# Optimization experiments

Hardware: AMD Instinct MI355X
Metric: run time of the kernel (lower is better)

Reference implementation:

```python
import jax, jax.numpy as jnp
import numpy as np

# dims
B, N, C_A, C_S, C_Z = 2, 8192, 128, 384, 16
H, D = 4, 32            # n_heads, head_dim (H*D == C_A)
NQ, NK = 32, 128        # local window: queries / keys
NB = 3                  # n_blocks
W = N // NQ             # number of query windows
HID = 2 * C_A           # transition expansion (n=2)


def _ln(x, eps=1e-5):
    # LayerNorm without affine params
    m = jnp.mean(x, axis=-1, keepdims=True)
    v = jnp.var(x, axis=-1, keepdims=True)
    return (x - m) * jax.lax.rsqrt(v + eps)


def setup_inputs() -> dict:
    key = jax.random.key(0)
    ks = iter(jax.random.split(key, 40))
    def rn(shape, scale=1.0):
        return jax.random.normal(next(ks), shape, dtype=jnp.float32) * jnp.float32(scale)
    inp = {
        'q': rn((B, N, C_A)),
        's': rn((B, N, C_S)),
        'p': rn((B, W, NQ, NK, C_Z)),
        # AttentionPairBias (AF3 Alg 24) params, stacked over blocks
        'adaln_scale_w': rn((NB, C_S, C_A), C_S ** -0.5),
        'adaln_scale_b': jnp.zeros((NB, C_A), jnp.float32),
        'adaln_shift_w': rn((NB, C_S, C_A), C_S ** -0.5),
        'wq': rn((NB, C_A, H * D), C_A ** -0.5),
        'bq': jnp.zeros((NB, H * D), jnp.float32),
        'wk': rn((NB, C_A, H * D), C_A ** -0.5),
        'wv': rn((NB, C_A, H * D), C_A ** -0.5),
        'lnz_w': jnp.ones((NB, C_Z), jnp.float32),
        'lnz_b': jnp.zeros((NB, C_Z), jnp.float32),
        'wb_pair': rn((NB, C_Z, H), C_Z ** -0.5),
        'wg': rn((NB, C_A, H * D), C_A ** -0.5),
        'wo': rn((NB, H * D, C_A), (H * D) ** -0.5),
        'sgate_w': rn((NB, C_S, C_A), C_S ** -0.5),
        'sgate_b': jnp.full((NB, C_A), -2.0, jnp.float32),
        # ConditionedTransitionBlock (AF3 Alg 25) params
        't_scale_w': rn((NB, C_S, C_A), C_S ** -0.5),
        't_scale_b': jnp.zeros((NB, C_A), jnp.float32),
        't_shift_w': rn((NB, C_S, C_A), C_S ** -0.5),
        't_wa': rn((NB, C_A, HID), C_A ** -0.5),
        't_wb': rn((NB, C_A, HID), C_A ** -0.5),
        't_wo': rn((NB, HID, C_A), HID ** -0.5),
        't_sgate_w': rn((NB, C_S, C_A), C_S ** -0.5),
        't_sgate_b': jnp.full((NB, C_A), -2.0, jnp.float32),
    }
    return inp


def reference(q, s, p,
              adaln_scale_w, adaln_scale_b, adaln_shift_w,
              wq, bq, wk, wv, lnz_w, lnz_b, wb_pair, wg, wo, sgate_w, sgate_b,
              t_scale_w, t_scale_b, t_shift_w, t_wa, t_wb, t_wo, t_sgate_w, t_sgate_b):
    a = q
    s_ln = _ln(s)  # [B, N, C_S], shared across blocks
    # local window key indices: window w covers queries [w*NQ, (w+1)*NQ), keys
    # are a centered NK-wide window -> offsets in [-(NK-NQ)//2, ...)
    off = (NK - NQ) // 2
    idx = jnp.arange(W)[:, None] * NQ - off + jnp.arange(NK)[None, :]  # [W, NK]
    valid = (idx >= 0) & (idx < N)
    idx_c = jnp.clip(idx, 0, N - 1)
    inv_sqrt_d = jnp.float32(1.0 / np.sqrt(D))
    NEG = jnp.float32(-1e9)

    for i in range(NB):
        # ---- AttentionPairBias (AdaLN-conditioned, pair-biased, gated) ----
        a_ln = _ln(a)
        a_ln = jax.nn.sigmoid(s_ln @ adaln_scale_w[i] + adaln_scale_b[i]) * a_ln \
               + s_ln @ adaln_shift_w[i]
        qh = (a_ln @ wq[i] + bq[i]).reshape(B, N, H, D)
        kh = (a_ln @ wk[i]).reshape(B, N, H, D)
        vh = (a_ln @ wv[i]).reshape(B, N, H, D)
        g = jax.nn.sigmoid(a_ln @ wg[i]).reshape(B, N, H, D)
        # pair bias from z: LN + linear to heads -> [B, W, NQ, NK, H]
        bias = (_ln(p) * lnz_w[i] + lnz_b[i]) @ wb_pair[i]
        qw = qh.reshape(B, W, NQ, H, D)
        kw = kh[:, idx_c]  # [B, W, NK, H, D]
        vw = vh[:, idx_c]
        logits = jnp.einsum('bwqhd,bwkhd->bwqkh', qw, kw) * inv_sqrt_d + bias
        logits = jnp.where(valid[None, :, None, :, None], logits, NEG)
        attn = jax.nn.softmax(logits, axis=3)
        ow = jnp.einsum('bwqkh,bwkhd->bwqhd', attn, vw)
        o = (g * ow.reshape(B, N, H, D)).reshape(B, N, H * D)
        attn_out = (o @ wo[i]) * jax.nn.sigmoid(s_ln @ sgate_w[i] + sgate_b[i])
        # ---- ConditionedTransitionBlock (SwiGLU, sigmoid-gated) ----
        t_ln = _ln(a)
        t_ln = jax.nn.sigmoid(s_ln @ t_scale_w[i] + t_scale_b[i]) * t_ln \
               + s_ln @ t_shift_w[i]
        hidden = jax.nn.silu(t_ln @ t_wa[i]) * (t_ln @ t_wb[i])
        trans_out = (hidden @ t_wo[i]) * jax.nn.sigmoid(s_ln @ t_sgate_w[i] + t_sgate_b[i])
        # AF3 Alg 23: a <- b + ConditionedTransitionBlock(a, s)
        a = attn_out + trans_out
    return a
```

## Files before the change

kernel.cpp:

```cpp
#include <hip/hip_runtime.h>
#include <hip/hip_bf16.h>
#include <cstddef>
#include <cstdint>

#define BB   2
#define NN   8192
#define CA   128
#define CS   384
#define CZ   16
#define HH   4
#define DD   32
#define NQW  32
#define NKW  128
#define NBLK 3
#define WW   256
#define MR   (BB*NN)
#define HIDN 256

typedef unsigned short u16;
typedef __attribute__((ext_vector_type(8))) short short8;
typedef __attribute__((ext_vector_type(4))) float floatx4;

__device__ __forceinline__ float sigmoidf_(float x) { return 1.f / (1.f + __expf(-x)); }

__device__ __forceinline__ u16 f2bf(float x) {
  unsigned u = __float_as_uint(x);
  unsigned r = (u + 0x7fffu + ((u >> 16) & 1u)) >> 16;
  return (u16)r;
}
__device__ __forceinline__ float bf2f(u16 u) {
  return __uint_as_float(((unsigned)u) << 16);
}

__device__ __forceinline__ void gload16(const u16* g, u16* l) {
  __builtin_amdgcn_global_load_lds(
      (const __attribute__((address_space(1))) unsigned int*)g,
      (__attribute__((address_space(3))) unsigned int*)l, 16, 0, 0);
}

__global__ __launch_bounds__(256) void ln_s_kernel(const float* __restrict__ s,
                                                   u16* __restrict__ s_ln_bf) {
  int row  = blockIdx.x * 4 + (threadIdx.x >> 6);
  int lane = threadIdx.x & 63;
  const float* sr = s + (size_t)row * CS;
  float x[6];
  float sum = 0.f, sq = 0.f;
#pragma unroll
  for (int t = 0; t < 6; ++t) { x[t] = sr[lane + 64*t]; sum += x[t]; sq += x[t]*x[t]; }
#pragma unroll
  for (int off = 32; off; off >>= 1) { sum += __shfl_down(sum, off); sq += __shfl_down(sq, off); }
  sum = __shfl(sum, 0); sq = __shfl(sq, 0);
  float mean = sum * (1.f/CS);
  float var  = sq  * (1.f/CS) - mean*mean;
  float rstd = rsqrtf(var + 1e-5f);
  u16* orow = s_ln_bf + (size_t)row * CS;
#pragma unroll
  for (int t = 0; t < 6; ++t) orow[lane + 64*t] = f2bf((x[t]-mean)*rstd);
}

__global__ __launch_bounds__(256) void modln_kernel(const float* __restrict__ a,
                                                    const u16* __restrict__ sp0,
                                                    const u16* __restrict__ sp1,
                                                    const u16* __restrict__ sp3,
                                                    const u16* __restrict__ sp4,
                                                    u16* __restrict__ amod,
                                                    u16* __restrict__ tmod) {
  int row  = blockIdx.x * 4 + (threadIdx.x >> 6);
  int lane = threadIdx.x & 63;
  const float* ar = a + (size_t)row * CA;
  float x0 = ar[lane], x1 = ar[lane + 64];
  float sum = x0 + x1, sq = x0*x0 + x1*x1;
#pragma unroll
  for (int off = 32; off; off >>= 1) { sum += __shfl_down(sum, off); sq += __shfl_down(sq, off); }
  sum = __shfl(sum, 0); sq = __shfl(sq, 0);
  float mean = sum * (1.f/CA);
  float var  = sq  * (1.f/CA) - mean*mean;
  float rstd = rsqrtf(var + 1e-5f);
  float n0 = (x0-mean)*rstd, n1 = (x1-mean)*rstd;
  size_t i0 = (size_t)row * CA + lane;
  amod[i0]      = f2bf(bf2f(sp0[i0])     *n0 + bf2f(sp1[i0]));
  amod[i0 + 64] = f2bf(bf2f(sp0[i0 + 64])*n1 + bf2f(sp1[i0 + 64]));
  tmod[i0]      = f2bf(bf2f(sp3[i0])     *n0 + bf2f(sp4[i0]));
  tmod[i0 + 64] = f2bf(bf2f(sp3[i0 + 64])*n1 + bf2f(sp4[i0 + 64]));
}

struct TJob { const float* src; u16* dst; int K; int N; };
struct TJobs { TJob j[42]; };

__global__ __launch_bounds__(256) void transpose_bf16(TJobs jobs) {
  TJob jb = jobs.j[blockIdx.z];
  int tk = blockIdx.x * 32, tn = blockIdx.y * 32;
  if (tk >= jb.K || tn >= jb.N) return;
  __shared__ float tile[32][33];
  int tx = threadIdx.x & 31;
  int ty = threadIdx.x >> 5;
#pragma unroll
  for (int r = ty; r < 32; r += 8) tile[r][tx] = jb.src[(size_t)(tk + r) * jb.N + tn + tx];
  __syncthreads();
#pragma unroll
  for (int r = ty; r < 32; r += 8)
    jb.dst[(size_t)(tn + r) * jb.K + tk + tx] = f2bf(tile[tx][r]);
}

struct GemmJob {
  const u16* A;
  const u16* Bt;
  const u16* Bt2;
  const float* bias;
  u16* outbf;
  int K;
  int ostride;
  int mode;
  int pad;
};
struct GemmJobs { GemmJob j[18]; };

template <bool DUAL>
__global__ __launch_bounds__(256) void gemm_mfma(GemmJobs jobs) {
  GemmJob jb = jobs.j[blockIdx.z];
  const int bm = blockIdx.y * 64, bn = blockIdx.x * 128;
  const int K = jb.K;

  __shared__ u16 As[2][2048];
  __shared__ u16 Bs[2][4096];
  __shared__ u16 Bs2[DUAL ? 2 : 1][DUAL ? 4096 : 8];

  const int tid  = threadIdx.x;
  const int lane = tid & 63;
  const int wave = tid >> 6;
  const int wr = wave >> 1, wc = wave & 1;
  const int l15 = lane & 15, quad = lane >> 4;

  floatx4 acc[2][4] = {};
  floatx4 acc2[DUAL ? 2 : 1][DUAL ? 4 : 1] = {};

  const u16* Ab   = jb.A  + ((size_t)bm + lane) * K + wave * 8;
  const u16* Bb0  = jb.Bt + ((size_t)bn + lane) * K + wave * 8;
  const u16* Bb1  = jb.Bt + ((size_t)bn + 64 + lane) * K + wave * 8;
  const u16* B2b0 = DUAL ? (jb.Bt2 + ((size_t)bn + lane) * K + wave * 8) : nullptr;
  const u16* B2b1 = DUAL ? (jb.Bt2 + ((size_t)bn + 64 + lane) * K + wave * 8) : nullptr;

  auto stage = [&](int k0, int pb) {
    gload16(Ab  + k0, As[pb] + wave * 512);
    gload16(Bb0 + k0, Bs[pb] + wave * 1024);
    gload16(Bb1 + k0, Bs[pb] + wave * 1024 + 512);
    if constexpr (DUAL) {
      gload16(B2b0 + k0, Bs2[pb] + wave * 1024);
      gload16(B2b1 + k0, Bs2[pb] + wave * 1024 + 512);
    }
  };

  stage(0, 0);
  __syncthreads();
  int cur = 0;
  for (int k0 = 0; k0 < K; k0 += 32) {
    if (k0 + 32 < K) stage(k0 + 32, cur ^ 1);

    short8 a_frag[2], b_frag[4];
#pragma unroll
    for (int mt = 0; mt < 2; ++mt)
      a_frag[mt] = *(const short8*)(As[cur] + quad * 512 + (wr * 32 + mt * 16 + l15) * 8);
#pragma unroll
    for (int nt = 0; nt < 4; ++nt)
      b_frag[nt] = *(const short8*)(Bs[cur] + quad * 1024 + (wc * 64 + nt * 16 + l15) * 8);
#pragma unroll
    for (int mt = 0; mt < 2; ++mt)
#pragma unroll
      for (int nt = 0; nt < 4; ++nt)
        acc[mt][nt] = __builtin_amdgcn_mfma_f32_16x16x32_bf16(a_frag[mt], b_frag[nt], acc[mt][nt], 0, 0, 0);
    if constexpr (DUAL) {
      short8 b2_frag[4];
#pragma unroll
      for (int nt = 0; nt < 4; ++nt)
        b2_frag[nt] = *(const short8*)(Bs2[cur] + quad * 1024 + (wc * 64 + nt * 16 + l15) * 8);
#pragma unroll
      for (int mt = 0; mt < 2; ++mt)
#pragma unroll
        for (int nt = 0; nt < 4; ++nt)
          acc2[mt][nt] = __builtin_amdgcn_mfma_f32_16x16x32_bf16(a_frag[mt], b2_frag[nt], acc2[mt][nt], 0, 0, 0);
    }
    __syncthreads();
    cur ^= 1;
  }

#pragma unroll
  for (int mt = 0; mt < 2; ++mt) {
#pragma unroll
    for (int nt = 0; nt < 4; ++nt) {
      int n = bn + wc * 64 + nt * 16 + l15;
      int mbase = bm + wr * 32 + mt * 16 + quad * 4;
      floatx4 v = acc[mt][nt];
      if constexpr (DUAL) {
        floatx4 v2 = acc2[mt][nt];
#pragma unroll
        for (int r = 0; r < 4; ++r) {
          size_t idx = (size_t)(mbase + r) * jb.ostride + n;
          float x1 = v[r];
          jb.outbf[idx] = f2bf(x1 * sigmoidf_(x1) * v2[r]);
        }
      } else if (jb.mode == 5) {
        int bidx = mbase >> 13;
        int tok  = mbase & (NN - 1);
        ushort4 o;
        o.x = f2bf(v[0]); o.y = f2bf(v[1]); o.z = f2bf(v[2]); o.w = f2bf(v[3]);
        *(ushort4*)(jb.outbf + (size_t)(bidx * CA + n) * NN + tok) = o;
      } else {
        float bias = jb.bias ? jb.bias[n] : 0.f;
#pragma unroll
        for (int r = 0; r < 4; ++r) {
          size_t idx = (size_t)(mbase + r) * jb.ostride + n;
          float x = v[r] + bias;
          jb.outbf[idx] = f2bf(jb.mode == 1 ? sigmoidf_(x) : x);
        }
      }
    }
  }
}

__global__ __launch_bounds__(256) void combo_kernel(const u16* __restrict__ O,
                                                    const u16* __restrict__ HID,
                                                    const u16* __restrict__ woT,
                                                    const u16* __restrict__ twoT,
                                                    const u16* __restrict__ g1,
                                                    const u16* __restrict__ g2,
                                                    float* __restrict__ outp) {
  const int bm = blockIdx.y * 64;
  __shared__ u16 As[2][2048];
  __shared__ u16 Bs[2][4096];
  const int tid  = threadIdx.x;
  const int lane = tid & 63;
  const int wave = tid >> 6;
  const int wr = wave >> 1, wc = wave & 1;
  const int l15 = lane & 15, quad = lane >> 4;

  floatx4 acc1[2][4] = {};
  floatx4 acc2[2][4] = {};

  const u16* A1  = O   + ((size_t)bm + lane) * CA + wave * 8;
  const u16* B10 = woT + ((size_t)lane) * CA + wave * 8;
  const u16* B11 = woT + ((size_t)64 + lane) * CA + wave * 8;
  const u16* A2  = HID  + ((size_t)bm + lane) * HIDN + wave * 8;
  const u16* B20 = twoT + ((size_t)lane) * HIDN + wave * 8;
  const u16* B21 = twoT + ((size_t)64 + lane) * HIDN + wave * 8;

  auto stage1 = [&](int k0, int pb) {
    gload16(A1  + k0, As[pb] + wave * 512);
    gload16(B10 + k0, Bs[pb] + wave * 1024);
    gload16(B11 + k0, Bs[pb] + wave * 1024 + 512);
  };
  auto stage2 = [&](int k0, int pb) {
    gload16(A2  + k0, As[pb] + wave * 512);
    gload16(B20 + k0, Bs[pb] + wave * 1024);
    gload16(B21 + k0, Bs[pb] + wave * 1024 + 512);
  };

  stage1(0, 0);
  __syncthreads();
  int cur = 0;
  for (int t = 0; t < 4; ++t) {
    if (t < 3) stage1((t + 1) * 32, cur ^ 1);
    else       stage2(0, cur ^ 1);
    short8 a_frag[2], b_frag[4];
#pragma unroll
    for (int mt = 0; mt < 2; ++mt)
      a_frag[mt] = *(const short8*)(As[cur] + quad * 512 + (wr * 32 + mt * 16 + l15) * 8);
#pragma unroll
    for (int nt = 0; nt < 4; ++nt)
      b_frag[nt] = *(const short8*)(Bs[cur] + quad * 1024 + (wc * 64 + nt * 16 + l15) * 8);
#pragma unroll
    for (int mt = 0; mt < 2; ++mt)
#pragma unroll
      for (int nt = 0; nt < 4; ++nt)
        acc1[mt][nt] = __builtin_amdgcn_mfma_f32_16x16x32_bf16(a_frag[mt], b_frag[nt], acc1[mt][nt], 0, 0, 0);
    __syncthreads();
    cur ^= 1;
  }
  for (int t = 0; t < 8; ++t) {
    if (t < 7) stage2((t + 1) * 32, cur ^ 1);
    short8 a_frag[2], b_frag[4];
#pragma unroll
    for (int mt = 0; mt < 2; ++mt)
      a_frag[mt] = *(const short8*)(As[cur] + quad * 512 + (wr * 32 + mt * 16 + l15) * 8);
#pragma unroll
    for (int nt = 0; nt < 4; ++nt)
      b_frag[nt] = *(const short8*)(Bs[cur] + quad * 1024 + (wc * 64 + nt * 16 + l15) * 8);
#pragma unroll
    for (int mt = 0; mt < 2; ++mt)
#pragma unroll
      for (int nt = 0; nt < 4; ++nt)
        acc2[mt][nt] = __builtin_amdgcn_mfma_f32_16x16x32_bf16(a_frag[mt], b_frag[nt], acc2[mt][nt], 0, 0, 0);
    __syncthreads();
    cur ^= 1;
  }

#pragma unroll
  for (int mt = 0; mt < 2; ++mt) {
#pragma unroll
    for (int nt = 0; nt < 4; ++nt) {
      int n = wc * 64 + nt * 16 + l15;
      int mbase = bm + wr * 32 + mt * 16 + quad * 4;
#pragma unroll
      for (int r = 0; r < 4; ++r) {
        size_t idx = (size_t)(mbase + r) * CA + n;
        outp[idx] = acc1[mt][nt][r] * bf2f(g1[idx]) + acc2[mt][nt][r] * bf2f(g2[idx]);
      }
    }
  }
}

__global__ __launch_bounds__(256) void bias3_kernel(const float* __restrict__ p,
                                                    const float* __restrict__ lnz_w,
                                                    const float* __restrict__ lnz_b,
                                                    const float* __restrict__ wb,
                                                    u16* __restrict__ biasT) {
  const int kc = blockIdx.x, w = blockIdx.y, b = blockIdx.z;
  __shared__ float effW[12][16];
  __shared__ float effb[12];
  const int t = threadIdx.x;
  if (t < 192) {
    int i = t >> 6, rem = t & 63, z = rem >> 2, hh = rem & 3;
    effW[i*4 + hh][z] = lnz_w[i*CZ + z] * wb[(i*CZ + z)*HH + hh];
  }
  if (t < 12) {
    int i = t >> 2, hh = t & 3;
    float acc = 0.f;
    for (int z = 0; z < 16; ++z) acc += lnz_b[i*CZ + z] * wb[(i*CZ + z)*HH + hh];
    effb[t] = acc;
  }
  __syncthreads();

  const int kk = t & 31, qg = (t >> 5) * 4;
  const int k = kc * 32 + kk;
  u16 out4[12][4];
#pragma unroll
  for (int r = 0; r < 4; ++r) {
    int qq = qg + r;
    const float4* pr = (const float4*)(p + (size_t)(((b * WW + w) * NQW + qq) * NKW + k) * 16);
    float4 p0 = pr[0], p1 = pr[1], p2 = pr[2], p3 = pr[3];
    float x[16] = {p0.x,p0.y,p0.z,p0.w, p1.x,p1.y,p1.z,p1.w,
                   p2.x,p2.y,p2.z,p2.w, p3.x,p3.y,p3.z,p3.w};
    float sum = 0.f, sq = 0.f;
#pragma unroll
    for (int z = 0; z < 16; ++z) { sum += x[z]; sq += x[z]*x[z]; }
    float mean = sum * (1.f/16.f);
    float var  = sq  * (1.f/16.f) - mean*mean;
    float rstd = rsqrtf(var + 1e-5f);
#pragma unroll
    for (int ih = 0; ih < 12; ++ih) {
      float acc = effb[ih];
#pragma unroll
      for (int z = 0; z < 16; ++z) acc += (x[z]-mean)*rstd * effW[ih][z];
      out4[ih][r] = f2bf(acc);
    }
  }
#pragma unroll
  for (int ih = 0; ih < 12; ++ih) {
    int i = ih >> 2, hh = ih & 3;
    u16* dst = biasT + ((((size_t)i * BB + b) * WW + w) * HH + hh) * 4096 + (size_t)k * 32 + qg;
    ushort4 uv; uv.x = out4[ih][0]; uv.y = out4[ih][1]; uv.z = out4[ih][2]; uv.w = out4[ih][3];
    *(ushort4*)dst = uv;
  }
}

__global__ __launch_bounds__(64) void attn_mfma(const u16* __restrict__ Qb,
                                                const u16* __restrict__ Kb,
                                                const u16* __restrict__ Vtb,
                                                const u16* __restrict__ Gb,
                                                const u16* __restrict__ biasT,
                                                u16* __restrict__ Ob) {
  const int w = blockIdx.x, h = blockIdx.y, b = blockIdx.z;
  __shared__ u16 Pt[128 * 36];
  __shared__ float inv_s[32];
  const int lane = threadIdx.x;
  const int l15 = lane & 15, quad = lane >> 4;
  const int tok0 = w * NQW - 48;

  short8 qf[2];
#pragma unroll
  for (int mt = 0; mt < 2; ++mt) {
    int qq = w * NQW + mt * 16 + l15;
    qf[mt] = *(const short8*)(Qb + (size_t)(b * NN + qq) * CA + h * DD + quad * 8);
  }
  floatx4 lg[2][8] = {};
#pragma unroll
  for (int nt = 0; nt < 8; ++nt) {
    int tk = tok0 + nt * 16 + l15;
    int tc = min(max(tk, 0), NN - 1);
    short8 kf = *(const short8*)(Kb + (size_t)(b * NN + tc) * CA + h * DD + quad * 8);
#pragma unroll
    for (int mt = 0; mt < 2; ++mt)
      lg[mt][nt] = __builtin_amdgcn_mfma_f32_16x16x32_bf16(qf[mt], kf, lg[mt][nt], 0, 0, 0);
  }

  const float scale = 0.17677669529663687f;
  const u16* bb = biasT + ((((size_t)b * WW + w) * HH + h) << 12);
  float mrow[2][4];
#pragma unroll
  for (int mt = 0; mt < 2; ++mt)
#pragma unroll
    for (int r = 0; r < 4; ++r) mrow[mt][r] = -3.0e38f;
#pragma unroll
  for (int nt = 0; nt < 8; ++nt) {
    int tk = tok0 + nt * 16 + l15;
    bool valid = (tk >= 0) && (tk < NN);
#pragma unroll
    for (int mt = 0; mt < 2; ++mt) {
      ushort4 bv = *(const ushort4*)(bb + (nt * 16 + l15) * 32 + mt * 16 + quad * 4);
      float bvf[4] = {bf2f(bv.x), bf2f(bv.y), bf2f(bv.z), bf2f(bv.w)};
#pragma unroll
      for (int r = 0; r < 4; ++r) {
        float l = valid ? (lg[mt][nt][r] * scale + bvf[r]) : -1e9f;
        lg[mt][nt][r] = l;
        mrow[mt][r] = fmaxf(mrow[mt][r], l);
      }
    }
  }
#pragma unroll
  for (int mt = 0; mt < 2; ++mt)
#pragma unroll
    for (int r = 0; r < 4; ++r) {
      float m = mrow[mt][r];
      m = fmaxf(m, __shfl_xor(m, 1));
      m = fmaxf(m, __shfl_xor(m, 2));
      m = fmaxf(m, __shfl_xor(m, 4));
      m = fmaxf(m, __shfl_xor(m, 8));
      mrow[mt][r] = m;
    }

  float srow[2][4] = {};
#pragma unroll
  for (int nt = 0; nt < 8; ++nt)
#pragma unroll
    for (int mt = 0; mt < 2; ++mt) {
      u16 pv[4];
#pragma unroll
      for (int r = 0; r < 4; ++r) {
        float e = __expf(lg[mt][nt][r] - mrow[mt][r]);
        srow[mt][r] += e;
        pv[r] = f2bf(e);
      }
      ushort4 uv; uv.x = pv[0]; uv.y = pv[1]; uv.z = pv[2]; uv.w = pv[3];
      *(ushort4*)(Pt + (nt * 16 + l15) * 36 + mt * 16 + quad * 4) = uv;
    }
#pragma unroll
  for (int mt = 0; mt < 2; ++mt)
#pragma unroll
    for (int r = 0; r < 4; ++r) {
      float ssum = srow[mt][r];
      ssum += __shfl_xor(ssum, 1);
      ssum += __shfl_xor(ssum, 2);
      ssum += __shfl_xor(ssum, 4);
      ssum += __shfl_xor(ssum, 8);
      if (l15 == 0) inv_s[mt * 16 + quad * 4 + r] = 1.f / ssum;
    }
  __syncthreads();

  floatx4 oacc[2][2] = {};
#pragma unroll
  for (int ks = 0; ks < 4; ++ks) {
    short8 pf[2];
#pragma unroll
    for (int ntq = 0; ntq < 2; ++ntq)
#pragma unroll
      for (int j = 0; j < 8; ++j)
        pf[ntq][j] = (short)Pt[(ks * 32 + quad * 8 + j) * 36 + ntq * 16 + l15];
    int tb = tok0 + ks * 32 + quad * 8;
    tb = min(max(tb, 0), NN - 8);
#pragma unroll
    for (int mtd = 0; mtd < 2; ++mtd) {
      short8 vf = *(const short8*)(Vtb + (size_t)(b * CA + h * DD + mtd * 16 + l15) * NN + tb);
#pragma unroll
      for (int ntq = 0; ntq < 2; ++ntq)
        oacc[mtd][ntq] = __builtin_amdgcn_mfma_f32_16x16x32_bf16(vf, pf[ntq], oacc[mtd][ntq], 0, 0, 0);
    }
  }

#pragma unroll
  for (int mtd = 0; mtd < 2; ++mtd)
#pragma unroll
    for (int ntq = 0; ntq < 2; ++ntq) {
      int qq = ntq * 16 + l15;
      float inv = inv_s[qq];
      int tok = w * NQW + qq;
      size_t base = (size_t)(b * NN + tok) * CA + h * DD + mtd * 16 + quad * 4;
      ushort4 gv = *(const ushort4*)(Gb + base);
      floatx4 v = oacc[mtd][ntq];
      ushort4 o;
      o.x = f2bf(bf2f(gv.x) * v[0] * inv);
      o.y = f2bf(bf2f(gv.y) * v[1] * inv);
      o.z = f2bf(bf2f(gv.z) * v[2] * inv);
      o.w = f2bf(bf2f(gv.w) * v[3] * inv);
      *(ushort4*)(Ob + base) = o;
    }
}

extern "C" void kernel_launch(void* const* d_in, const int* in_sizes, int n_in,
                              void* d_out, int out_size, void* d_ws, size_t ws_size,
                              hipStream_t stream) {
  const float* q             = (const float*)d_in[0];
  const float* s             = (const float*)d_in[1];
  const float* p             = (const float*)d_in[2];
  const float* adaln_scale_w = (const float*)d_in[3];
  const float* adaln_scale_b = (const float*)d_in[4];
  const float* adaln_shift_w = (const float*)d_in[5];
  const float* wq            = (const float*)d_in[6];
  const float* bq            = (const float*)d_in[7];
  const float* wk            = (const float*)d_in[8];
  const float* wv            = (const float*)d_in[9];
  const float* lnz_w         = (const float*)d_in[10];
  const float* lnz_b         = (const float*)d_in[11];
  const float* wb_pair       = (const float*)d_in[12];
  const float* wg            = (const float*)d_in[13];
  const float* wo            = (const float*)d_in[14];
  const float* sgate_w       = (const float*)d_in[15];
  const float* sgate_b       = (const float*)d_in[16];
  const float* t_scale_w     = (const float*)d_in[17];
  const float* t_scale_b     = (const float*)d_in[18];
  const float* t_shift_w     = (const float*)d_in[19];
  const float* t_wa          = (const float*)d_in[20];
  const float* t_wb          = (const float*)d_in[21];
  const float* t_wo          = (const float*)d_in[22];
  const float* t_sgate_w     = (const float*)d_in[23];
  const float* t_sgate_b     = (const float*)d_in[24];
  float* out = (float*)d_out;

  const size_t MC = (size_t)MR * CA;
  float* fws   = (float*)d_ws;
  float* abuf0 = fws;
  float* abuf1 = abuf0 + MC;
  u16* uws     = (u16*)(abuf1 + MC);
  u16* s_ln_bf = uws;
  u16* SP      = s_ln_bf + (size_t)MR * CS;
  u16* amod    = SP + 18*MC;
  u16* tmod    = amod + MC;
  u16* Qb      = tmod + MC;
  u16* Kb      = Qb + MC;
  u16* Vtb     = Kb + MC;
  u16* Gb      = Vtb + MC;
  u16* Ob      = Gb + MC;
  u16* HIDb    = Ob + MC;
  u16* biasT   = HIDb + 2*MC;
  u16* wbuf    = biasT + (size_t)3*BB*WW*HH*NQW*NKW;

  const size_t WBLK = 6*(size_t)CA*CS + 5*(size_t)CA*CA + 3*(size_t)CA*HIDN;
  const size_t o_ascale = 0;
  const size_t o_ashift = o_ascale + (size_t)CA*CS;
  const size_t o_sgate  = o_ashift + (size_t)CA*CS;
  const size_t o_tscale = o_sgate  + (size_t)CA*CS;
  const size_t o_tshift = o_tscale + (size_t)CA*CS;
  const size_t o_tsgate = o_tshift + (size_t)CA*CS;
  const size_t o_wq     = o_tsgate + (size_t)CA*CS;
  const size_t o_wk     = o_wq + (size_t)CA*CA;
  const size_t o_wv     = o_wk + (size_t)CA*CA;
  const size_t o_wg     = o_wv + (size_t)CA*CA;
  const size_t o_wo     = o_wg + (size_t)CA*CA;
  const size_t o_twa    = o_wo + (size_t)CA*CA;
  const size_t o_twb    = o_twa + (size_t)HIDN*CA;
  const size_t o_two    = o_twb + (size_t)HIDN*CA;

  ln_s_kernel<<<MR/4, 256, 0, stream>>>(s, s_ln_bf);

  TJobs tj;
  for (int i = 0; i < NBLK; ++i) {
    u16* wb0 = wbuf + (size_t)i * WBLK;
    int b14 = i * 14;
    tj.j[b14+0]  = TJob{adaln_scale_w + (size_t)i*CS*CA, wb0 + o_ascale, CS, CA};
    tj.j[b14+1]  = TJob{adaln_shift_w + (size_t)i*CS*CA, wb0 + o_ashift, CS, CA};
    tj.j[b14+2]  = TJob{sgate_w       + (size_t)i*CS*CA, wb0 + o_sgate,  CS, CA};
    tj.j[b14+3]  = TJob{t_scale_w     + (size_t)i*CS*CA, wb0 + o_tscale, CS, CA};
    tj.j[b14+4]  = TJob{t_shift_w     + (size_t)i*CS*CA, wb0 + o_tshift, CS, CA};
    tj.j[b14+5]  = TJob{t_sgate_w     + (size_t)i*CS*CA, wb0 + o_tsgate, CS, CA};
    tj.j[b14+6]  = TJob{wq   + (size_t)i*CA*CA,   wb0 + o_wq,  CA, CA};
    tj.j[b14+7]  = TJob{wk   + (size_t)i*CA*CA,   wb0 + o_wk,  CA, CA};
    tj.j[b14+8]  = TJob{wv   + (size_t)i*CA*CA,   wb0 + o_wv,  CA, CA};
    tj.j[b14+9]  = TJob{wg   + (size_t)i*CA*CA,   wb0 + o_wg,  CA, CA};
    tj.j[b14+10] = TJob{wo   + (size_t)i*CA*CA,   wb0 + o_wo,  CA, CA};
    tj.j[b14+11] = TJob{t_wa + (size_t)i*CA*HIDN, wb0 + o_twa, CA, HIDN};
    tj.j[b14+12] = TJob{t_wb + (size_t)i*CA*HIDN, wb0 + o_twb, CA, HIDN};
    tj.j[b14+13] = TJob{t_wo + (size_t)i*HIDN*CA, wb0 + o_two, HIDN, CA};
  }
  transpose_bf16<<<dim3(12, 8, 42), 256, 0, stream>>>(tj);

  bias3_kernel<<<dim3(4, WW, BB), 256, 0, stream>>>(p, lnz_w, lnz_b, wb_pair, biasT);

  {
    GemmJobs js = {};
    for (int i = 0; i < NBLK; ++i) {
      u16* wb0 = wbuf + (size_t)i * WBLK;
      js.j[i*6+0] = GemmJob{s_ln_bf, wb0 + o_ascale, nullptr, adaln_scale_b + i*CA, SP + (i*6+0)*MC, CS, CA, 1, 0};
      js.j[i*6+1] = GemmJob{s_ln_bf, wb0 + o_ashift, nullptr, nullptr,              SP + (i*6+1)*MC, CS, CA, 0, 0};
      js.j[i*6+2] = GemmJob{s_ln_bf, wb0 + o_sgate,  nullptr, sgate_b   + i*CA,     SP + (i*6+2)*MC, CS, CA, 1, 0};
      js.j[i*6+3] = GemmJob{s_ln_bf, wb0 + o_tscale, nullptr, t_scale_b + i*CA,     SP + (i*6+3)*MC, CS, CA, 1, 0};
      js.j[i*6+4] = GemmJob{s_ln_bf, wb0 + o_tshift, nullptr, nullptr,              SP + (i*6+4)*MC, CS, CA, 0, 0};
      js.j[i*6+5] = GemmJob{s_ln_bf, wb0 + o_tsgate, nullptr, t_sgate_b + i*CA,     SP + (i*6+5)*MC, CS, CA, 1, 0};
    }
    gemm_mfma<false><<<dim3(1, MR/64, 18), 256, 0, stream>>>(js);
  }

  for (int i = 0; i < NBLK; ++i) {
    const float* a_in = (i == 0) ? q : (i == 1 ? abuf0 : abuf1);
    float* a_out = (i == 2) ? out : (i == 0 ? abuf0 : abuf1);
    u16* wb0 = wbuf + (size_t)i * WBLK;

    modln_kernel<<<MR/4, 256, 0, stream>>>(a_in, SP + (i*6+0)*MC, SP + (i*6+1)*MC,
                                           SP + (i*6+3)*MC, SP + (i*6+4)*MC, amod, tmod);

    GemmJobs jq = {};
    jq.j[0] = GemmJob{amod, wb0 + o_wq, nullptr, bq + i*CA, Qb,  CA, CA, 0, 0};
    jq.j[1] = GemmJob{amod, wb0 + o_wk, nullptr, nullptr,   Kb,  CA, CA, 0, 0};
    jq.j[2] = GemmJob{amod, wb0 + o_wv, nullptr, nullptr,   Vtb, CA, CA, 5, 0};
    jq.j[3] = GemmJob{amod, wb0 + o_wg, nullptr, nullptr,   Gb,  CA, CA, 1, 0};
    gemm_mfma<false><<<dim3(1, MR/64, 4), 256, 0, stream>>>(jq);

    GemmJobs jh = {};
    jh.j[0] = GemmJob{tmod, wb0 + o_twa, wb0 + o_twb, nullptr, HIDb, CA, HIDN, 4, 0};
    gemm_mfma<true><<<dim3(2, MR/64, 1), 256, 0, stream>>>(jh);

    attn_mfma<<<dim3(WW, HH, BB), 64, 0, stream>>>(
        Qb, Kb, Vtb, Gb, biasT + (size_t)i * BB*WW*HH*4096, Ob);

    combo_kernel<<<dim3(1, MR/64), 256, 0, stream>>>(
        Ob, HIDb, wb0 + o_wo, wb0 + o_two,
        SP + (i*6+2)*MC, SP + (i*6+5)*MC, a_out);
  }
}
```

Before: 590.6 us.

## Enlarge GEMM M-tile and share A tile across multiple jobs; overlap combo GEMMs

The batched GEMM kernel now uses 128-row M tiles and processes J jobs that share the same A operand in one block, so the A tile is loaded into LDS once and reused across several weight matrices. This cuts redundant global reads of the activation matrix. The combo kernel double-buffers both GEMM operand sets separately and interleaves the two K loops, which reduces the number of barrier iterations. The larger accumulator arrays (up to 48 floatx4 per thread for J=3) and LDS raise register and LDS pressure, which may reduce occupancy or cause spills.

Result: slower. 637.8 us (+8.0%).

```diff
diff --git a/kernel.cpp b/kernel.cpp
--- a/kernel.cpp
+++ b/kernel.cpp
@@ -115,14 +115,15 @@
 };
 struct GemmJobs { GemmJob j[18]; };
 
-template <bool DUAL>
+template <int J, bool DUAL>
 __global__ __launch_bounds__(256) void gemm_mfma(GemmJobs jobs) {
-  GemmJob jb = jobs.j[blockIdx.z];
-  const int bm = blockIdx.y * 64, bn = blockIdx.x * 128;
-  const int K = jb.K;
-
-  __shared__ u16 As[2][2048];
-  __shared__ u16 Bs[2][4096];
+  const int jbase = blockIdx.z * J;
+  const GemmJob jb0 = jobs.j[jbase];
+  const int bm = blockIdx.y * 128, bn = blockIdx.x * 128;
+  const int K = jb0.K;
+
+  __shared__ u16 As[2][4096];
+  __shared__ u16 Bs[2][J][4096];
   __shared__ u16 Bs2[DUAL ? 2 : 1][DUAL ? 4096 : 8];
 
   const int tid  = threadIdx.x;
@@ -131,19 +132,30 @@
   const int wr = wave >> 1, wc = wave & 1;
   const int l15 = lane & 15, quad = lane >> 4;
 
-  floatx4 acc[2][4] = {};
-  floatx4 acc2[DUAL ? 2 : 1][DUAL ? 4 : 1] = {};
-
-  const u16* Ab   = jb.A  + ((size_t)bm + lane) * K + wave * 8;
-  const u16* Bb0  = jb.Bt + ((size_t)bn + lane) * K + wave * 8;
-  const u16* Bb1  = jb.Bt + ((size_t)bn + 64 + lane) * K + wave * 8;
-  const u16* B2b0 = DUAL ? (jb.Bt2 + ((size_t)bn + lane) * K + wave * 8) : nullptr;
-  const u16* B2b1 = DUAL ? (jb.Bt2 + ((size_t)bn + 64 + lane) * K + wave * 8) : nullptr;
+  floatx4 acc[J][4][4] = {};
+  floatx4 acc2[DUAL ? 4 : 1][DUAL ? 4 : 1] = {};
+
+  const u16* Ab0 = jb0.A + ((size_t)bm + lane) * K + wave * 8;
+  const u16* Ab1 = jb0.A + ((size_t)bm + 64 + lane) * K + wave * 8;
+  const u16* Bb0[J];
+  const u16* Bb1[J];
+#pragma unroll
+  for (int jj = 0; jj < J; ++jj) {
+    const u16* Bt = jobs.j[jbase + jj].Bt;
+    Bb0[jj] = Bt + ((size_t)bn + lane) * K + wave * 8;
+    Bb1[jj] = Bt + ((size_t)bn + 64 + lane) * K + wave * 8;
+  }
+  const u16* B2b0 = DUAL ? (jb0.Bt2 + ((size_t)bn + lane) * K + wave * 8) : nullptr;
+  const u16* B2b1 = DUAL ? (jb0.Bt2 + ((size_t)bn + 64 + lane) * K + wave * 8) : nullptr;
 
   auto stage = [&](int k0, int pb) {
-    gload16(Ab  + k0, As[pb] + wave * 512);
-    gload16(Bb0 + k0, Bs[pb] + wave * 1024);
-    gload16(Bb1 + k0, Bs[pb] + wave * 1024 + 512);
+    gload16(Ab0 + k0, As[pb] + wave * 1024);
+    gload16(Ab1 + k0, As[pb] + wave * 1024 + 512);
+#pragma unroll
+    for (int jj = 0; jj < J; ++jj) {
+      gload16(Bb0[jj] + k0, Bs[pb][jj] + wave * 1024);
+      gload16(Bb1[jj] + k0, Bs[pb][jj] + wave * 1024 + 512);
+    }
     if constexpr (DUAL) {
       gload16(B2b0 + k0, Bs2[pb] + wave * 1024);
       gload16(B2b1 + k0, Bs2[pb] + wave * 1024 + 512);
@@ -156,25 +168,29 @@
   for (int k0 = 0; k0 < K; k0 += 32) {
     if (k0 + 32 < K) stage(k0 + 32, cur ^ 1);
 
-    short8 a_frag[2], b_frag[4];
-#pragma unroll
-    for (int mt = 0; mt < 2; ++mt)
-      a_frag[mt] = *(const short8*)(As[cur] + quad * 512 + (wr * 32 + mt * 16 + l15) * 8);
-#pragma unroll
-    for (int nt = 0; nt < 4; ++nt)
-      b_frag[nt] = *(const short8*)(Bs[cur] + quad * 1024 + (wc * 64 + nt * 16 + l15) * 8);
-#pragma unroll
-    for (int mt = 0; mt < 2; ++mt)
+    short8 a_frag[4];
+#pragma unroll
+    for (int mt = 0; mt < 4; ++mt)
+      a_frag[mt] = *(const short8*)(As[cur] + quad * 1024 + (wr * 64 + mt * 16 + l15) * 8);
+#pragma unroll
+    for (int jj = 0; jj < J; ++jj) {
+      short8 b_frag[4];
 #pragma unroll
       for (int nt = 0; nt < 4; ++nt)
-        acc[mt][nt] = __builtin_amdgcn_mfma_f32_16x16x32_bf16(a_frag[mt], b_frag[nt], acc[mt][nt], 0, 0, 0);
+        b_frag[nt] = *(const short8*)(Bs[cur][jj] + quad * 1024 + (wc * 64 + nt * 16 + l15) * 8);
+#pragma unroll
+      for (int mt = 0; mt < 4; ++mt)
+#pragma unroll
+        for (int nt = 0; nt < 4; ++nt)
+          acc[jj][mt][nt] = __builtin_amdgcn_mfma_f32_16x16x32_bf16(a_frag[mt], b_frag[nt], acc[jj][mt][nt], 0, 0, 0);
+    }
     if constexpr (DUAL) {
       short8 b2_frag[4];
 #pragma unroll
       for (int nt = 0; nt < 4; ++nt)
         b2_frag[nt] = *(const short8*)(Bs2[cur] + quad * 1024 + (wc * 64 + nt * 16 + l15) * 8);
 #pragma unroll
-      for (int mt = 0; mt < 2; ++mt)
+      for (int mt = 0; mt < 4; ++mt)
 #pragma unroll
         for (int nt = 0; nt < 4; ++nt)
           acc2[mt][nt] = __builtin_amdgcn_mfma_f32_16x16x32_bf16(a_frag[mt], b2_frag[nt], acc2[mt][nt], 0, 0, 0);
@@ -184,33 +200,37 @@
   }
 
 #pragma unroll
-  for (int mt = 0; mt < 2; ++mt) {
-#pragma unroll
-    for (int nt = 0; nt < 4; ++nt) {
-      int n = bn + wc * 64 + nt * 16 + l15;
-      int mbase = bm + wr * 32 + mt * 16 + quad * 4;
-      floatx4 v = acc[mt][nt];
-      if constexpr (DUAL) {
-        floatx4 v2 = acc2[mt][nt];
-#pragma unroll
-        for (int r = 0; r < 4; ++r) {
-          size_t idx = (size_t)(mbase + r) * jb.ostride + n;
-          float x1 = v[r];
-          jb.outbf[idx] = f2bf(x1 * sigmoidf_(x1) * v2[r]);
-        }
-      } else if (jb.mode == 5) {
-        int bidx = mbase >> 13;
-        int tok  = mbase & (NN - 1);
-        ushort4 o;
-        o.x = f2bf(v[0]); o.y = f2bf(v[1]); o.z = f2bf(v[2]); o.w = f2bf(v[3]);
-        *(ushort4*)(jb.outbf + (size_t)(bidx * CA + n) * NN + tok) = o;
-      } else {
-        float bias = jb.bias ? jb.bias[n] : 0.f;
-#pragma unroll
-        for (int r = 0; r < 4; ++r) {
-          size_t idx = (size_t)(mbase + r) * jb.ostride + n;
-          float x = v[r] + bias;
-          jb.outbf[idx] = f2bf(jb.mode == 1 ? sigmoidf_(x) : x);
+  for (int jj = 0; jj < J; ++jj) {
+    GemmJob jb = jobs.j[jbase + jj];
+#pragma unroll
+    for (int mt = 0; mt < 4; ++mt) {
+#pragma unroll
+      for (int nt = 0; nt < 4; ++nt) {
+        int n = bn + wc * 64 + nt * 16 + l15;
+        int mbase = bm + wr * 64 + mt * 16 + quad * 4;
+        floatx4 v = acc[jj][mt][nt];
+        if constexpr (DUAL) {
+          floatx4 v2 = acc2[mt][nt];
+#pragma unroll
+          for (int r = 0; r < 4; ++r) {
+            size_t idx = (size_t)(mbase + r) * jb.ostride + n;
+            float x1 = v[r];
+            jb.outbf[idx] = f2bf(x1 * sigmoidf_(x1) * v2[r]);
+          }
+        } else if (jb.mode == 5) {
+          int bidx = mbase >> 13;
+          int tok  = mbase & (NN - 1);
+          ushort4 o;
+          o.x = f2bf(v[0]); o.y = f2bf(v[1]); o.z = f2bf(v[2]); o.w = f2bf(v[3]);
+          *(ushort4*)(jb.outbf + (size_t)(bidx * CA + n) * NN + tok) = o;
+        } else {
+          float bias = jb.bias ? jb.bias[n] : 0.f;
+#pragma unroll
+          for (int r = 0; r < 4; ++r) {
+            size_t idx = (size_t)(mbase + r) * jb.ostride + n;
+            float x = v[r] + bias;
+            jb.outbf[idx] = f2bf(jb.mode == 1 ? sigmoidf_(x) : x);
+          }
         }
       }
     }
@@ -225,8 +245,10 @@
                                                     const u16* __restrict__ g2,
                                                     float* __restrict__ outp) {
   const int bm = blockIdx.y * 64;
-  __shared__ u16 As[2][2048];
-  __shared__ u16 Bs[2][4096];
+  __shared__ u16 As1[2][2048];
+  __shared__ u16 Bs1[2][4096];
+  __shared__ u16 As2[2][2048];
+  __shared__ u16 Bs2h[2][4096];
   const int tid  = threadIdx.x;
   const int lane = tid & 63;
   const int wave = tid >> 6;
@@ -236,59 +258,60 @@
   floatx4 acc1[2][4] = {};
   floatx4 acc2[2][4] = {};
 
-  const u16* A1  = O   + ((size_t)bm + lane) * CA + wave * 8;
-  const u16* B10 = woT + ((size_t)lane) * CA + wave * 8;
-  const u16* B11 = woT + ((size_t)64 + lane) * CA + wave * 8;
+  const u16* A1  = O    + ((size_t)bm + lane) * CA + wave * 8;
+  const u16* B10 = woT  + ((size_t)lane) * CA + wave * 8;
+  const u16* B11 = woT  + ((size_t)64 + lane) * CA + wave * 8;
   const u16* A2  = HID  + ((size_t)bm + lane) * HIDN + wave * 8;
   const u16* B20 = twoT + ((size_t)lane) * HIDN + wave * 8;
   const u16* B21 = twoT + ((size_t)64 + lane) * HIDN + wave * 8;
 
   auto stage1 = [&](int k0, int pb) {
-    gload16(A1  + k0, As[pb] + wave * 512);
-    gload16(B10 + k0, Bs[pb] + wave * 1024);
-    gload16(B11 + k0, Bs[pb] + wave * 1024 + 512);
+    gload16(A1  + k0, As1[pb] + wave * 512);
+    gload16(B10 + k0, Bs1[pb] + wave * 1024);
+    gload16(B11 + k0, Bs1[pb] + wave * 1024 + 512);
   };
   auto stage2 = [&](int k0, int pb) {
-    gload16(A2  + k0, As[pb] + wave * 512);
-    gload16(B20 + k0, Bs[pb] + wave * 1024);
-    gload16(B21 + k0, Bs[pb] + wave * 1024 + 512);
+    gload16(A2  + k0, As2[pb] + wave * 512);
+    gload16(B20 + k0, Bs2h[pb] + wave * 1024);
+    gload16(B21 + k0, Bs2h[pb] + wave * 1024 + 512);
   };
 
   stage1(0, 0);
+  stage2(0, 0);
   __syncthreads();
   int cur = 0;
-  for (int t = 0; t < 4; ++t) {
-    if (t < 3) stage1((t + 1) * 32, cur ^ 1);
-    else       stage2(0, cur ^ 1);
-    short8 a_frag[2], b_frag[4];
-#pragma unroll
-    for (int mt = 0; mt < 2; ++mt)
-      a_frag[mt] = *(const short8*)(As[cur] + quad * 512 + (wr * 32 + mt * 16 + l15) * 8);
-#pragma unroll
-    for (int nt = 0; nt < 4; ++nt)
-      b_frag[nt] = *(const short8*)(Bs[cur] + quad * 1024 + (wc * 64 + nt * 16 + l15) * 8);
-#pragma unroll
-    for (int mt = 0; mt < 2; ++mt)
+  for (int t = 0; t < 8; ++t) {
+    if (t + 1 < 4) stage1((t + 1) * 32, cur ^ 1);
+    if (t + 1 < 8) stage2((t + 1) * 32, cur ^ 1);
+
+    if (t < 4) {
+      short8 a_frag[2], b_frag[4];
+#pragma unroll
+      for (int mt = 0; mt < 2; ++mt)
+        a_frag[mt] = *(const short8*)(As1[cur] + quad * 512 + (wr * 32 + mt * 16 + l15) * 8);
 #pragma unroll
       for (int nt = 0; nt < 4; ++nt)
-        acc1[mt][nt] = __builtin_amdgcn_mfma_f32_16x16x32_bf16(a_frag[mt], b_frag[nt], acc1[mt][nt], 0, 0, 0);
-    __syncthreads();
-    cur ^= 1;
-  }
-  for (int t = 0; t < 8; ++t) {
-    if (t < 7) stage2((t + 1) * 32, cur ^ 1);
-    short8 a_frag[2], b_frag[4];
-#pragma unroll
-    for (int mt = 0; mt < 2; ++mt)
-      a_frag[mt] = *(const short8*)(As[cur] + quad * 512 + (wr * 32 + mt * 16 + l15) * 8);
-#pragma unroll
-    for (int nt = 0; nt < 4; ++nt)
-      b_frag[nt] = *(const short8*)(Bs[cur] + quad * 1024 + (wc * 64 + nt * 16 + l15) * 8);
-#pragma unroll
-    for (int mt = 0; mt < 2; ++mt)
+        b_frag[nt] = *(const short8*)(Bs1[cur] + quad * 1024 + (wc * 64 + nt * 16 + l15) * 8);
+#pragma unroll
+      for (int mt = 0; mt < 2; ++mt)
+#pragma unroll
+        for (int nt = 0; nt < 4; ++nt)
+          acc1[mt][nt] = __builtin_amdgcn_mfma_f32_16x16x32_bf16(a_frag[mt], b_frag[nt], acc1[mt][nt], 0, 0, 0);
+    }
+    {
+      short8 a_frag[2], b_frag[4];
+#pragma unroll
+      for (int mt = 0; mt < 2; ++mt)
+        a_frag[mt] = *(const short8*)(As2[cur] + quad * 512 + (wr * 32 + mt * 16 + l15) * 8);
 #pragma unroll
       for (int nt = 0; nt < 4; ++nt)
-        acc2[mt][nt] = __builtin_amdgcn_mfma_f32_16x16x32_bf16(a_frag[mt], b_frag[nt], acc2[mt][nt], 0, 0, 0);
+        b_frag[nt] = *(const short8*)(Bs2h[cur] + quad * 1024 + (wc * 64 + nt * 16 + l15) * 8);
+#pragma unroll
+      for (int mt = 0; mt < 2; ++mt)
+#pragma unroll
+        for (int nt = 0; nt < 4; ++nt)
+          acc2[mt][nt] = __builtin_amdgcn_mfma_f32_16x16x32_bf16(a_frag[mt], b_frag[nt], acc2[mt][nt], 0, 0, 0);
+    }
     __syncthreads();
     cur ^= 1;
   }
@@ -594,7 +617,7 @@
       js.j[i*6+4] = GemmJob{s_ln_bf, wb0 + o_tshift, nullptr, nullptr,              SP + (i*6+4)*MC, CS, CA, 0, 0};
       js.j[i*6+5] = GemmJob{s_ln_bf, wb0 + o_tsgate, nullptr, t_sgate_b + i*CA,     SP + (i*6+5)*MC, CS, CA, 1, 0};
     }
-    gemm_mfma<false><<<dim3(1, MR/64, 18), 256, 0, stream>>>(js);
+    gemm_mfma<3, false><<<dim3(1, MR/128, 6), 256, 0, stream>>>(js);
   }
 
   for (int i = 0; i < NBLK; ++i) {
@@ -610,11 +633,11 @@
     jq.j[1] = GemmJob{amod, wb0 + o_wk, nullptr, nullptr,   Kb,  CA, CA, 0, 0};
     jq.j[2] = GemmJob{amod, wb0 + o_wv, nullptr, nullptr,   Vtb, CA, CA, 5, 0};
     jq.j[3] = GemmJob{amod, wb0 + o_wg, nullptr, nullptr,   Gb,  CA, CA, 1, 0};
-    gemm_mfma<false><<<dim3(1, MR/64, 4), 256, 0, stream>>>(jq);
+    gemm_mfma<2, false><<<dim3(1, MR/128, 2), 256, 0, stream>>>(jq);
 
     GemmJobs jh = {};
     jh.j[0] = GemmJob{tmod, wb0 + o_twa, wb0 + o_twb, nullptr, HIDb, CA, HIDN, 4, 0};
-    gemm_mfma<true><<<dim3(2, MR/64, 1), 256, 0, stream>>>(jh);
+    gemm_mfma<1, true><<<dim3(2, MR/128, 1), 256, 0, stream>>>(jh);
 
     attn_mfma<<<dim3(WW, HH, BB), 64, 0, stream>>>(
         Qb, Kb, Vtb, Gb, biasT + (size_t)i * BB*WW*HH*4096, Ob);
```
